# Performance work log

Measured on AMD Instinct MI355X. Metric: run time of the kernel, lower is better.

The kernel has to match this reference:

```python
import jax, jax.numpy as jnp
import numpy as np

EPS = 1e-12  # F.normalize default eps


def _l2_normalize(x, axis):
    n = jnp.sqrt(jnp.sum(x * x, axis=axis, keepdims=True))
    return x / jnp.maximum(n, EPS)


def setup_inputs() -> dict:
    key = jax.random.key(0)
    k1, k2 = jax.random.split(key)
    code = jax.random.normal(k1, (8, 768, 32, 32), dtype=jnp.float32)
    clusters = jax.random.normal(k2, (64, 768), dtype=jnp.float32)
    return {"code": code, "clusters": clusters, "image_hw": 512}


def reference(code, clusters, image_hw):
    # L2-normalize cluster centroids over channel dim and features over C
    normed_clusters = _l2_normalize(clusters, axis=1)            # [N, C]
    normed_features = _l2_normalize(code, axis=1)                # [B, C, H, W]
    # cosine similarity to every cluster
    inner_products = jnp.einsum('bchw,nc->bnhw', normed_features, normed_clusters)  # [B,N,H,W]
    # hard nearest-cluster assignment -> one-hot over N (channel axis 1)
    assign = jnp.argmax(inner_products, axis=1)                  # [B, H, W] int
    n_classes = clusters.shape[0]
    cluster_probs = jnp.moveaxis(
        jax.nn.one_hot(assign, n_classes, dtype=jnp.float32), -1, 1)  # [B,N,H,W]
    # training loss: negative mean of selected (max) similarity
    cluster_loss = -jnp.mean(jnp.sum(cluster_probs * inner_products, axis=1))
    # resize_to(cluster_probs, image): bilinear upsample to image resolution
    B, N = cluster_probs.shape[0], cluster_probs.shape[1]
    resized = jax.image.resize(cluster_probs, (B, N, image_hw, image_hw), method='bilinear')
    return (cluster_loss, resized, code)
```

## Files before the change

### kernel.cpp

```cpp
#include <hip/hip_runtime.h>

#define CCH 768
#define NCL 64
#define HWIN 1024
#define RES_ELEMS 134217728LL
#define CODE_ELEMS 6291456LL
#define CQUADS 1572863LL
#define COPY_BLOCKS 1536
#define DENSE_BLOCKS 4096

__global__ __launch_bounds__(256) void k_norm(const float* __restrict__ clusters,
                                              const float* __restrict__ code,
                                              float* __restrict__ nc_t,
                                              float* __restrict__ out)
{
    int tid = threadIdx.x;
    int n = blockIdx.x;
    __shared__ float red[256];
    float v0 = clusters[n * CCH + tid];
    float v1 = clusters[n * CCH + tid + 256];
    float v2 = clusters[n * CCH + tid + 512];
    red[tid] = v0 * v0 + v1 * v1 + v2 * v2;
    __syncthreads();
    for (int off = 128; off > 0; off >>= 1) {
        if (tid < off) red[tid] += red[tid + off];
        __syncthreads();
    }
    float scale = 1.0f / fmaxf(sqrtf(red[0]), 1e-12f);
    nc_t[(tid      ) * NCL + n] = v0 * scale;
    nc_t[(tid + 256) * NCL + n] = v1 * scale;
    nc_t[(tid + 512) * NCL + n] = v2 * scale;
    if (n == 0 && tid == 0) {
        out[0] = 0.0f;
        out[RES_ELEMS + 1] = code[0];
        out[RES_ELEMS + 2] = code[1];
        out[RES_ELEMS + 3] = code[2];
        out[RES_ELEMS + CODE_ELEMS] = code[CODE_ELEMS - 1];
    }
}

__global__ __launch_bounds__(256) void k_assign(const float* __restrict__ code,
                                                const float* __restrict__ nc_t,
                                                int* __restrict__ assign,
                                                float* __restrict__ out)
{
    __shared__ float lds_nc[64 * 64];
    __shared__ float lds_red[8 * 2048];
    __shared__ float lds_sq[8 * 32];

    int tid = threadIdx.x;
    int blk = blockIdx.x;
    int cg = tid >> 5;
    int ng = (tid >> 3) & 3;
    int pg = tid & 7;
    int b = blk >> 5;
    int pixb = (blk & 31) << 5;
    const float* codeB = code + (size_t)b * CCH * HWIN + pixb + (pg << 2);

    float acc[4][16];
    #pragma unroll
    for (int p = 0; p < 4; ++p)
        #pragma unroll
        for (int q = 0; q < 16; ++q) acc[p][q] = 0.f;
    float sq0 = 0.f, sq1 = 0.f, sq2 = 0.f, sq3 = 0.f;

    for (int k = 0; k < 12; ++k) {
        __syncthreads();
        const float4* src = (const float4*)(nc_t + k * 4096);
        float4* dst = (float4*)lds_nc;
        #pragma unroll
        for (int i = 0; i < 4; ++i) dst[tid + 256 * i] = src[tid + 256 * i];
        __syncthreads();
        #pragma unroll
        for (int m = 0; m < 8; ++m) {
            int ch = k * 64 + cg * 8 + m;
            float4 f = *(const float4*)(codeB + ch * HWIN);
            sq0 += f.x * f.x; sq1 += f.y * f.y; sq2 += f.z * f.z; sq3 += f.w * f.w;
            const float* ncrow = lds_nc + ((cg * 8 + m) << 6) + (ng << 4);
            #pragma unroll
            for (int q = 0; q < 16; ++q) {
                float w = ncrow[q];
                acc[0][q] += f.x * w;
                acc[1][q] += f.y * w;
                acc[2][q] += f.z * w;
                acc[3][q] += f.w * w;
            }
        }
    }

    #pragma unroll
    for (int p = 0; p < 4; ++p) {
        float4* dstp = (float4*)&lds_red[cg * 2048 + (pg * 4 + p) * 64 + ng * 16];
        dstp[0] = make_float4(acc[p][0],  acc[p][1],  acc[p][2],  acc[p][3]);
        dstp[1] = make_float4(acc[p][4],  acc[p][5],  acc[p][6],  acc[p][7]);
        dstp[2] = make_float4(acc[p][8],  acc[p][9],  acc[p][10], acc[p][11]);
        dstp[3] = make_float4(acc[p][12], acc[p][13], acc[p][14], acc[p][15]);
    }
    if (ng == 0) {
        lds_sq[cg * 32 + pg * 4 + 0] = sq0;
        lds_sq[cg * 32 + pg * 4 + 1] = sq1;
        lds_sq[cg * 32 + pg * 4 + 2] = sq2;
        lds_sq[cg * 32 + pg * 4 + 3] = sq3;
    }
    __syncthreads();

    for (int idx = tid; idx < 2048; idx += 256) {
        float s = 0.f;
        #pragma unroll
        for (int c2 = 0; c2 < 8; ++c2) s += lds_red[c2 * 2048 + idx];
        lds_nc[idx] = s;
    }
    __syncthreads();

    if (tid < 32) {
        float ss = 0.f;
        #pragma unroll
        for (int c2 = 0; c2 < 8; ++c2) ss += lds_sq[c2 * 32 + tid];
        float inv = 1.0f / fmaxf(sqrtf(ss), 1e-12f);
        float best = -1e30f; int bi = 0;
        for (int n = 0; n < 64; ++n) {
            float v = lds_nc[tid * 64 + n];
            if (v > best) { best = v; bi = n; }
        }
        assign[blk * 32 + tid] = bi;
        float l = best * inv;
        l += __shfl_down(l, 16);
        l += __shfl_down(l, 8);
        l += __shfl_down(l, 4);
        l += __shfl_down(l, 2);
        l += __shfl_down(l, 1);
        if (tid == 0) atomicAdd(out, -l * (1.0f / 8192.0f));
    }
}

__global__ __launch_bounds__(256) void k_dense(const int* __restrict__ assign,
                                               const float* __restrict__ code,
                                               float* __restrict__ out)
{
    int tid = threadIdx.x;
    int blk = blockIdx.x;

    if (blk >= DENSE_BLOCKS) {
        long long u = (long long)(blk - DENSE_BLOCKS) * 256 + tid;
        #pragma unroll
        for (int k = 0; k < 4; ++k) {
            long long q = u + (long long)k * (COPY_BLOCKS * 256);
            if (q < CQUADS) {
                const float* src = code + 3 + 4 * q;
                float4 v = make_float4(src[0], src[1], src[2], src[3]);
                *(float4*)(out + RES_ELEMS + 4 + 4 * q) = v;
            }
        }
        return;
    }

    int b = blk >> 9;
    int i = blk & 511;
    __shared__ int   s_r0[32], s_r1[32];
    __shared__ int4  s_ids[128];
    __shared__ float4 s_fj[128];

    float xi = (i + 0.5f) * 0.0625f - 0.5f;
    float fif = floorf(xi);
    int ii = (int)fif;
    float fi = xi - fif;
    int i0 = ii < 0 ? 0 : ii;
    int i1 = (ii + 1) > 31 ? 31 : (ii + 1);

    if (tid < 32) {
        s_r0[tid] = assign[(b << 10) + (i0 << 5) + tid];
        s_r1[tid] = assign[(b << 10) + (i1 << 5) + tid];
    }
    __syncthreads();

    if (tid < 128) {
        int s = tid;
        int4 ids; float4 fj4;
        int jl[4];
        if (s == 0) { jl[0] = 0; jl[1] = 1; jl[2] = 2; jl[3] = 511; }
        else { jl[0] = 4 * s - 1; jl[1] = 4 * s; jl[2] = 4 * s + 1; jl[3] = 4 * s + 2; }
        int pk[4]; float fjv[4];
        #pragma unroll
        for (int k = 0; k < 4; ++k) {
            int j = jl[k];
            float xj = (j + 0.5f) * 0.0625f - 0.5f;
            float fjf = floorf(xj);
            int jj = (int)fjf;
            fjv[k] = xj - fjf;
            int j0 = jj < 0 ? 0 : jj;
            int j1 = (jj + 1) > 31 ? 31 : (jj + 1);
            pk[k] = s_r0[j0] | (s_r0[j1] << 8) | (s_r1[j0] << 16) | (s_r1[j1] << 24);
        }
        ids.x = pk[0]; ids.y = pk[1]; ids.z = pk[2]; ids.w = pk[3];
        fj4.x = fjv[0]; fj4.y = fjv[1]; fj4.z = fjv[2]; fj4.w = fjv[3];
        s_ids[s] = ids;
        s_fj[s] = fj4;
    }
    __syncthreads();

    float fi1 = 1.0f - fi;
    long long rowoff = 1LL + ((long long)b << 24) + ((long long)i << 9);

    #pragma unroll 4
    for (int it = 0; it < 32; ++it) {
        int task = it * 256 + tid;
        int n = task >> 7;
        int s = task & 127;
        int4 p4 = s_ids[s];
        float4 f4 = s_fj[s];
        float v[4];
        int pks[4] = { p4.x, p4.y, p4.z, p4.w };
        float fjs[4] = { f4.x, f4.y, f4.z, f4.w };
        #pragma unroll
        for (int k = 0; k < 4; ++k) {
            int p = pks[k];
            float P = (((p      ) & 255) == n ? fi1 : 0.f)
                    + (((p >> 16) & 255) == n ? fi  : 0.f);
            float Q = (((p >>  8) & 255) == n ? fi1 : 0.f)
                    + (((p >> 24) & 255) == n ? fi  : 0.f);
            v[k] = P + fjs[k] * (Q - P);
        }
        float* rowbase = out + rowoff + ((long long)n << 18);
        if (s == 0) {
            rowbase[0] = v[0]; rowbase[1] = v[1]; rowbase[2] = v[2]; rowbase[511] = v[3];
        } else {
            *(float4*)(rowbase + 4 * s - 1) = make_float4(v[0], v[1], v[2], v[3]);
        }
    }
}

extern "C" void kernel_launch(void* const* d_in, const int* in_sizes, int n_in,
                              void* d_out, int out_size, void* d_ws, size_t ws_size,
                              hipStream_t stream)
{
    const float* code     = (const float*)d_in[0];
    const float* clusters = (const float*)d_in[1];
    float* out = (float*)d_out;
    float* nc_t = (float*)d_ws;
    int* assign = (int*)((char*)d_ws + 196608);

    k_norm  <<<NCL,                       256, 0, stream>>>(clusters, code, nc_t, out);
    k_assign<<<256,                       256, 0, stream>>>(code, nc_t, assign, out);
    k_dense <<<DENSE_BLOCKS + COPY_BLOCKS, 256, 0, stream>>>(assign, code, out);
}
```

Before: 640.3 us.

## Restructure dense upsample kernel to process 8 rows per block across all classes

The bilinear one-hot upsample kernel now assigns 8 output rows per block (512 blocks instead of 4096). Each block stages the whole per-batch assignment map in LDS, precomputes packed neighbor ids once per pixel group, and then loops over all 64 classes with the per-thread data kept in registers. This amortizes index setup and LDS traffic across more output, at the cost of fewer blocks, more registers and a longer serial loop per thread. The output size is 512 MB, so the kernel stays bound by store bandwidth.

```diff
diff --git a/kernel.cpp b/kernel.cpp
--- a/kernel.cpp
+++ b/kernel.cpp
@@ -7,7 +7,7 @@
 #define CODE_ELEMS 6291456LL
 #define CQUADS 1572863LL
 #define COPY_BLOCKS 1536
-#define DENSE_BLOCKS 4096
+#define DENSE2_BLOCKS 512
 
 __global__ __launch_bounds__(256) void k_norm(const float* __restrict__ clusters,
                                               const float* __restrict__ code,
@@ -133,15 +133,15 @@
     }
 }
 
-__global__ __launch_bounds__(256) void k_dense(const int* __restrict__ assign,
-                                               const float* __restrict__ code,
-                                               float* __restrict__ out)
+__global__ __launch_bounds__(256) void k_dense2(const int* __restrict__ assign,
+                                                const float* __restrict__ code,
+                                                float* __restrict__ out)
 {
     int tid = threadIdx.x;
     int blk = blockIdx.x;
 
-    if (blk >= DENSE_BLOCKS) {
-        long long u = (long long)(blk - DENSE_BLOCKS) * 256 + tid;
+    if (blk >= DENSE2_BLOCKS) {
+        long long u = (long long)(blk - DENSE2_BLOCKS) * 256 + tid;
         #pragma unroll
         for (int k = 0; k < 4; ++k) {
             long long q = u + (long long)k * (COPY_BLOCKS * 256);
@@ -154,32 +154,35 @@
         return;
     }
 
-    int b = blk >> 9;
-    int i = blk & 511;
-    __shared__ int   s_r0[32], s_r1[32];
-    __shared__ int4  s_ids[128];
-    __shared__ float4 s_fj[128];
-
-    float xi = (i + 0.5f) * 0.0625f - 0.5f;
-    float fif = floorf(xi);
-    int ii = (int)fif;
-    float fi = xi - fif;
-    int i0 = ii < 0 ? 0 : ii;
-    int i1 = (ii + 1) > 31 ? 31 : (ii + 1);
-
-    if (tid < 32) {
-        s_r0[tid] = assign[(b << 10) + (i0 << 5) + tid];
-        s_r1[tid] = assign[(b << 10) + (i1 << 5) + tid];
-    }
-    __syncthreads();
-
+    int b  = blk >> 6;
+    int ic = blk & 63;
+
+    __shared__ int    s_as[1024] __attribute__((aligned(16)));
+    __shared__ int4   s_jp[128];
+    __shared__ float4 s_fj4[128];
+    __shared__ int4   s_pk[1024];
+    __shared__ float  s_fi[8], s_fi1[8];
+    __shared__ int    s_i0[8], s_i1[8];
+
+    *(int4*)&s_as[tid * 4] = *(const int4*)&assign[(b << 10) + tid * 4];
+
+    if (tid < 8) {
+        int i = ic * 8 + tid;
+        float xi = (i + 0.5f) * 0.0625f - 0.5f;
+        float fif = floorf(xi);
+        int ii = (int)fif;
+        float fi = xi - fif;
+        s_fi[tid] = fi;
+        s_fi1[tid] = 1.0f - fi;
+        s_i0[tid] = (ii < 0 ? 0 : ii) << 5;
+        s_i1[tid] = ((ii + 1) > 31 ? 31 : (ii + 1)) << 5;
+    }
     if (tid < 128) {
         int s = tid;
-        int4 ids; float4 fj4;
         int jl[4];
         if (s == 0) { jl[0] = 0; jl[1] = 1; jl[2] = 2; jl[3] = 511; }
         else { jl[0] = 4 * s - 1; jl[1] = 4 * s; jl[2] = 4 * s + 1; jl[3] = 4 * s + 2; }
-        int pk[4]; float fjv[4];
+        int jp[4]; float fjv[4];
         #pragma unroll
         for (int k = 0; k < 4; ++k) {
             int j = jl[k];
@@ -189,42 +192,78 @@
             fjv[k] = xj - fjf;
             int j0 = jj < 0 ? 0 : jj;
             int j1 = (jj + 1) > 31 ? 31 : (jj + 1);
-            pk[k] = s_r0[j0] | (s_r0[j1] << 8) | (s_r1[j0] << 16) | (s_r1[j1] << 24);
-        }
-        ids.x = pk[0]; ids.y = pk[1]; ids.z = pk[2]; ids.w = pk[3];
-        fj4.x = fjv[0]; fj4.y = fjv[1]; fj4.z = fjv[2]; fj4.w = fjv[3];
-        s_ids[s] = ids;
-        s_fj[s] = fj4;
-    }
-    __syncthreads();
-
-    float fi1 = 1.0f - fi;
-    long long rowoff = 1LL + ((long long)b << 24) + ((long long)i << 9);
-
-    #pragma unroll 4
-    for (int it = 0; it < 32; ++it) {
+            jp[k] = j0 | (j1 << 16);
+        }
+        s_jp[s]  = make_int4(jp[0], jp[1], jp[2], jp[3]);
+        s_fj4[s] = make_float4(fjv[0], fjv[1], fjv[2], fjv[3]);
+    }
+    __syncthreads();
+
+    #pragma unroll
+    for (int e4 = 0; e4 < 4; ++e4) {
+        int e = e4 * 256 + tid;
+        int r = e >> 7;
+        int s = e & 127;
+        int4 jp4 = s_jp[s];
+        const int* r0 = s_as + s_i0[r];
+        const int* r1 = s_as + s_i1[r];
+        int jpk[4] = { jp4.x, jp4.y, jp4.z, jp4.w };
+        int pk[4];
+        #pragma unroll
+        for (int k = 0; k < 4; ++k) {
+            int j0 = jpk[k] & 0xffff;
+            int j1 = jpk[k] >> 16;
+            pk[k] = r0[j0] | (r0[j1] << 8) | (r1[j0] << 16) | (r1[j1] << 24);
+        }
+        s_pk[e] = make_int4(pk[0], pk[1], pk[2], pk[3]);
+    }
+    __syncthreads();
+
+    int4   P[4];
+    float4 F[4];
+    float  FI[4], FI1[4];
+    long long OFF[4];
+    bool   HEAD[4];
+    #pragma unroll
+    for (int it = 0; it < 4; ++it) {
         int task = it * 256 + tid;
-        int n = task >> 7;
+        int r = task >> 7;
         int s = task & 127;
-        int4 p4 = s_ids[s];
-        float4 f4 = s_fj[s];
-        float v[4];
-        int pks[4] = { p4.x, p4.y, p4.z, p4.w };
-        float fjs[4] = { f4.x, f4.y, f4.z, f4.w };
-        #pragma unroll
-        for (int k = 0; k < 4; ++k) {
-            int p = pks[k];
-            float P = (((p      ) & 255) == n ? fi1 : 0.f)
-                    + (((p >> 16) & 255) == n ? fi  : 0.f);
-            float Q = (((p >>  8) & 255) == n ? fi1 : 0.f)
-                    + (((p >> 24) & 255) == n ? fi  : 0.f);
-            v[k] = P + fjs[k] * (Q - P);
-        }
-        float* rowbase = out + rowoff + ((long long)n << 18);
-        if (s == 0) {
-            rowbase[0] = v[0]; rowbase[1] = v[1]; rowbase[2] = v[2]; rowbase[511] = v[3];
-        } else {
-            *(float4*)(rowbase + 4 * s - 1) = make_float4(v[0], v[1], v[2], v[3]);
+        P[it]   = s_pk[task];
+        F[it]   = s_fj4[s];
+        FI[it]  = s_fi[r];
+        FI1[it] = s_fi1[r];
+        HEAD[it] = (s == 0);
+        OFF[it] = ((long long)r << 9) + (HEAD[it] ? 0 : (4 * s - 1));
+    }
+
+    long long base = 1LL + ((long long)b << 24) + ((long long)(ic * 8) << 9);
+
+    for (int n = 0; n < 64; ++n) {
+        float* pbase = out + base + ((long long)n << 18);
+        #pragma unroll
+        for (int it = 0; it < 4; ++it) {
+            int4 p4 = P[it];
+            float4 f4 = F[it];
+            float fi = FI[it], fi1 = FI1[it];
+            int pks[4] = { p4.x, p4.y, p4.z, p4.w };
+            float fjs[4] = { f4.x, f4.y, f4.z, f4.w };
+            float v[4];
+            #pragma unroll
+            for (int k = 0; k < 4; ++k) {
+                int p = pks[k];
+                float Pv = (((p      ) & 255) == n ? fi1 : 0.f)
+                         + (((p >> 16) & 255) == n ? fi  : 0.f);
+                float Qv = (((p >>  8) & 255) == n ? fi1 : 0.f)
+                         + (((p >> 24) & 255) == n ? fi  : 0.f);
+                v[k] = Pv + fjs[k] * (Qv - Pv);
+            }
+            float* dst = pbase + OFF[it];
+            if (HEAD[it]) {
+                dst[0] = v[0]; dst[1] = v[1]; dst[2] = v[2]; dst[511] = v[3];
+            } else {
+                *(float4*)dst = make_float4(v[0], v[1], v[2], v[3]);
+            }
         }
     }
 }
@@ -239,7 +278,7 @@
     float* nc_t = (float*)d_ws;
     int* assign = (int*)((char*)d_ws + 196608);
 
-    k_norm  <<<NCL,                       256, 0, stream>>>(clusters, code, nc_t, out);
-    k_assign<<<256,                       256, 0, stream>>>(code, nc_t, assign, out);
-    k_dense <<<DENSE_BLOCKS + COPY_BLOCKS, 256, 0, stream>>>(assign, code, out);
-}
+    k_norm   <<<NCL,                         256, 0, stream>>>(clusters, code, nc_t, out);
+    k_assign <<<256,                         256, 0, stream>>>(code, nc_t, assign, out);
+    k_dense2 <<<DENSE2_BLOCKS + COPY_BLOCKS, 256, 0, stream>>>(assign, code, out);
+}
```

Measured after the change: 683.2 us. 1.07x slower.
